# Kernel optimization log

Hardware: AMD Instinct MI355X
Metric: run time of the kernel (lower is better)

## Reference

```python
import jax, jax.numpy as jnp
import numpy as np

B, N, C = 4, 2048, 512
H = 8  # num_heads
HD = C // H  # head_dim = 64


def setup_inputs() -> dict:
    key = jax.random.key(0)
    k_x, k_qkv, k_w, k_b = jax.random.split(key, 4)
    x = jax.random.normal(k_x, (B, N, C), dtype=jnp.float32)
    # torch nn.Linear weights are stored as (out_features, in_features)
    w_qkv = jax.random.normal(k_qkv, (3 * C, C), dtype=jnp.float32) * 0.02  # bias=False
    w_proj = jax.random.normal(k_w, (C, C), dtype=jnp.float32) * 0.02
    b_proj = jax.random.normal(k_b, (C,), dtype=jnp.float32) * 0.02
    return {"x": x, "w_qkv": w_qkv, "w_proj": w_proj, "b_proj": b_proj}


def reference(x, w_qkv, w_proj, b_proj):
    b, n, c = x.shape
    scale = HD ** -0.5
    # QKV projection (no bias): (B,N,C) @ (C,3C) -> (B,N,3C)
    qkv = jnp.einsum('bnc,dc->bnd', x, w_qkv)
    qkv = qkv.reshape(b, n, 3, H, HD).transpose(2, 0, 3, 1, 4)  # (3,B,H,N,HD)
    q, k, v = qkv[0], qkv[1], qkv[2]
    # scaled dot-product attention, full N x N scores
    attn = jnp.einsum('bhqd,bhkd->bhqk', q, k) * scale
    attn = jax.nn.softmax(attn, axis=-1)
    out = jnp.einsum('bhqk,bhkd->bhqd', attn, v)  # (B,H,N,HD)
    out = out.transpose(0, 2, 1, 3).reshape(b, n, c)  # (B,N,C)
    # output projection with bias
    return jnp.einsum('bnc,dc->bnd', out, w_proj) + b_proj
```

## Files before the change

### kernel.cpp

```cpp
#include <hip/hip_runtime.h>

typedef _Float16 f16;
typedef _Float16 f16x4 __attribute__((ext_vector_type(4)));
typedef _Float16 f16x8 __attribute__((ext_vector_type(8)));
typedef __fp16 fp16x2 __attribute__((ext_vector_type(2)));
typedef float f32x4 __attribute__((ext_vector_type(4)));

static __device__ __forceinline__ f32x4 mfma_k32(f16x8 a, f16x8 b, f32x4 c) {
  return __builtin_amdgcn_mfma_f32_16x16x32_f16(a, b, c, 0, 0, 0);
}
static __device__ __forceinline__ f32x4 mfma_k16(f16x4 a, f16x4 b, f32x4 c) {
  return __builtin_amdgcn_mfma_f32_16x16x16f16(a, b, c, 0, 0, 0);
}
static __device__ __forceinline__ void gll16(const f16* g, f16* l) {
  __builtin_amdgcn_global_load_lds(
      (const __attribute__((address_space(1))) void*)g,
      (__attribute__((address_space(3))) void*)l, 16, 0, 0);
}

#define BN 2048
#define CC 512
#define NHD 64
#define MROWS 8192
#define SLAB ((size_t)32 * BN * NHD)
#define CH 64
#define QSCALE 0.1803368801111204f

__global__ __launch_bounds__(256)
void cvt_f16(const float* __restrict__ X, const float* __restrict__ Wq,
             const float* __restrict__ Wp, f16* __restrict__ x16,
             f16* __restrict__ wq16, f16* __restrict__ wp16) {
  const int idx = blockIdx.x * 256 + threadIdx.x;
  const int stride = gridDim.x * 256;
  for (int i = idx; i < (MROWS * CC) / 4; i += stride) {
    float4 v = ((const float4*)X)[i];
    f16x4 h = {(f16)v.x, (f16)v.y, (f16)v.z, (f16)v.w};
    ((f16x4*)x16)[i] = h;
  }
  for (int i = idx; i < (3 * CC * CC) / 4; i += stride) {
    float4 v = ((const float4*)Wq)[i];
    f16x4 h = {(f16)v.x, (f16)v.y, (f16)v.z, (f16)v.w};
    ((f16x4*)wq16)[i] = h;
  }
  for (int i = idx; i < (CC * CC) / 4; i += stride) {
    float4 v = ((const float4*)Wp)[i];
    f16x4 h = {(f16)v.x, (f16)v.y, (f16)v.z, (f16)v.w};
    ((f16x4*)wp16)[i] = h;
  }
}

__global__ __launch_bounds__(256)
void qkv_gemm(const f16* __restrict__ X, const f16* __restrict__ W,
              f16* __restrict__ qkv) {
  __shared__ __align__(16) f16 As[128 * 32];
  __shared__ __align__(16) f16 Bs[128 * 32];
  __shared__ __align__(16) f16 ep[64 * 130];
  const int t = threadIdx.x;
  const int lane = t & 63, wave = t >> 6;
  const int wr = wave >> 1, wc = wave & 1;
  const int mt = blockIdx.x / 12, nt = blockIdx.x % 12;
  const int m0 = mt * 128, n0 = nt * 128;
  const int grp = lane >> 4, lid = lane & 15;

  const int srow = 32 * wave + (lane >> 2);
  const int gslot = (lane & 3) ^ ((lane >> 2) & 3);
  const int ga0 = (m0 + srow) * CC + gslot * 8;
  const int gb0 = (n0 + srow) * CC + gslot * 8;
  f16* const ldsA = As + wave * 1024;
  f16* const ldsB = Bs + wave * 1024;

  const int abase = wr * 2048 + lid * 32 + (grp ^ (lid & 3)) * 8;
  const int bbase = wc * 2048 + lid * 32 + (grp ^ (lid & 3)) * 8;

  const f32x4 zf = {0.f, 0.f, 0.f, 0.f};
  f32x4 acc[4][4];
#pragma unroll
  for (int i = 0; i < 4; i++)
#pragma unroll
    for (int j = 0; j < 4; j++) acc[i][j] = zf;

  for (int k0 = 0; k0 < CC; k0 += 32) {
    gll16(X + ga0 + k0, ldsA);
    gll16(X + ga0 + 16 * CC + k0, ldsA + 512);
    gll16(W + gb0 + k0, ldsB);
    gll16(W + gb0 + 16 * CC + k0, ldsB + 512);
    __syncthreads();
    f16x8 af[4], bf[4];
#pragma unroll
    for (int mi = 0; mi < 4; mi++)
      af[mi] = *(const f16x8*)&As[abase + mi * 512];
#pragma unroll
    for (int ni = 0; ni < 4; ni++)
      bf[ni] = *(const f16x8*)&Bs[bbase + ni * 512];
#pragma unroll
    for (int mi = 0; mi < 4; mi++)
#pragma unroll
      for (int ni = 0; ni < 4; ni++)
        acc[mi][ni] = mfma_k32(af[mi], bf[ni], acc[mi][ni]);
    __syncthreads();
  }

  const int s = n0 >> 9;
  if (s == 2) {
#pragma unroll
    for (int ni = 0; ni < 4; ni++) {
      int d = n0 + wc * 64 + ni * 16 + lid;
      int h = (d & 511) >> 6;
      int hd = d & 63;
#pragma unroll
      for (int mi = 0; mi < 4; mi++) {
        int row0 = m0 + wr * 64 + mi * 16 + grp * 4;
        int b = row0 >> 11, nA = row0 & 2047;
        int posA = (nA & ~31) | (((nA >> 2) & 3) << 3) | (((nA >> 4) & 1) << 2);
        f16x4 pk = {(f16)acc[mi][ni][0], (f16)acc[mi][ni][1],
                    (f16)acc[mi][ni][2], (f16)acc[mi][ni][3]};
        *(f16x4*)&qkv[2 * SLAB + ((size_t)((b * 8 + h) * 64 + hd)) * BN + posA] = pk;
      }
    }
  } else {
    const float scale = (s == 0) ? QSCALE : 1.0f;
#pragma unroll
    for (int ph = 0; ph < 2; ++ph) {
      if (wr == ph) {
#pragma unroll
        for (int mi = 0; mi < 4; mi++)
#pragma unroll
          for (int ni = 0; ni < 4; ni++)
#pragma unroll
            for (int i = 0; i < 4; i++)
              ep[(mi * 16 + grp * 4 + i) * 130 + wc * 64 + ni * 16 + lid] =
                  (f16)(acc[mi][ni][i] * scale);
      }
      __syncthreads();
#pragma unroll
      for (int u = 0; u < 4; ++u) {
        int unit = t + u * 256;
        int row = unit >> 4, seg = unit & 15;
        int row_g = m0 + ph * 64 + row;
        int b = row_g >> 11, n = row_g & 2047;
        int d_g = n0 + seg * 8;
        int h = (d_g & 511) >> 6, hd = d_g & 63;
        f16x8 v = *(const f16x8*)&ep[row * 130 + seg * 8];
        *(f16x8*)&qkv[(size_t)s * SLAB + ((size_t)((b * 8 + h) * BN + n)) * 64 + hd] = v;
      }
      __syncthreads();
    }
  }
}

__global__ __launch_bounds__(256)
void attn(const f16* __restrict__ qkv, f16* __restrict__ O) {
  __shared__ __align__(16) char smem[32768];

  const int bh = blockIdx.x & 31;
  const int qb = blockIdx.x >> 5;
  const f16* Q = qkv + (size_t)bh * BN * NHD;
  const f16* K = qkv + SLAB + (size_t)bh * BN * NHD;
  const f16* VT = qkv + 2 * SLAB + (size_t)bh * (size_t)NHD * BN;
  const int t = threadIdx.x, lane = t & 63, wave = t >> 6;
  const int grp = lane >> 4, qv = lane & 15;
  const int qrow = qb * 64 + wave * 16 + qv;
  const int xr = (qv & 7) << 4;

  char* const kaddr0 = smem + qv * 128 + ((grp * 16) ^ xr);
  char* const kaddr1 = smem + qv * 128 + ((grp * 16 + 64) ^ xr);

  const int srow = wave * 16 + (lane >> 3);
  const int scol = (lane & 7) ^ (lane >> 3);
  const int lo_k0 = srow * NHD + scol * 8;
  const int lo_k1 = (srow + 8) * NHD + scol * 8;
  const int lo_v0 = srow * BN + scol * 8;
  const int lo_v1 = (srow + 8) * BN + scol * 8;
  f16* const dK = (f16*)(smem + wave * 2048);
  f16* const dV = (f16*)(smem + 16384 + wave * 2048);

  f16x8 qf0 = *(const f16x8*)(Q + (size_t)qrow * NHD + grp * 8);
  f16x8 qf1 = *(const f16x8*)(Q + (size_t)qrow * NHD + 32 + grp * 8);

  const f32x4 zf = {0.f, 0.f, 0.f, 0.f};
  const f16x4 ones = {(f16)1.f, (f16)1.f, (f16)1.f, (f16)1.f};
  f32x4 acc[4];
#pragma unroll
  for (int i = 0; i < 4; i++) acc[i] = zf;
  f32x4 lacc = zf;

  int koff = 0, voff = 0;
  gll16(K + lo_k0, dK);
  gll16(K + lo_k1, dK + 512);
  gll16(VT + lo_v0, dV);
  gll16(VT + lo_v1, dV + 512);
  koff = CH * NHD; voff = CH;
  __syncthreads();

#define ATTN_BODY(BUF, PF)                                                    \
  {                                                                           \
    if (PF) {                                                                 \
      gll16(K + koff + lo_k0, dK + (BUF ^ 1) * 4096);                         \
      gll16(K + koff + lo_k1, dK + (BUF ^ 1) * 4096 + 512);                   \
      gll16(VT + voff + lo_v0, dV + (BUF ^ 1) * 4096);                        \
      gll16(VT + voff + lo_v1, dV + (BUF ^ 1) * 4096 + 512);                  \
      koff += CH * NHD; voff += CH;                                           \
    }                                                                         \
    __builtin_amdgcn_s_setprio(1);                                            \
    _Pragma("unroll")                                                         \
    for (int kt2 = 0; kt2 < 2; kt2++) {                                       \
      char* const ka = kt2 ? kaddr1 : kaddr0;                                 \
      f16x8 k0a = *(const f16x8*)(kaddr0 + BUF * 8192 + kt2 * 4096);          \
      f16x8 k1a = *(const f16x8*)(kaddr1 + BUF * 8192 + kt2 * 4096);          \
      f32x4 st0 = mfma_k32(k1a, qf1, mfma_k32(k0a, qf0, zf));                 \
      f16x8 k0b = *(const f16x8*)(kaddr0 + BUF * 8192 + kt2 * 4096 + 2048);   \
      f16x8 k1b = *(const f16x8*)(kaddr1 + BUF * 8192 + kt2 * 4096 + 2048);   \
      f32x4 st1 = mfma_k32(k1b, qf1, mfma_k32(k0b, qf0, zf));                 \
      union { f16x4 v; fp16x2 h[2]; } u0, u1;                                 \
      u0.h[0] = __builtin_amdgcn_cvt_pkrtz(exp2f(st0[0]), exp2f(st0[1]));     \
      u0.h[1] = __builtin_amdgcn_cvt_pkrtz(exp2f(st0[2]), exp2f(st0[3]));     \
      u1.h[0] = __builtin_amdgcn_cvt_pkrtz(exp2f(st1[0]), exp2f(st1[1]));     \
      u1.h[1] = __builtin_amdgcn_cvt_pkrtz(exp2f(st1[2]), exp2f(st1[3]));     \
      f16x4 pb0 = u0.v, pb1 = u1.v;                                           \
      lacc = mfma_k16(ones, pb0, lacc);                                       \
      lacc = mfma_k16(ones, pb1, lacc);                                       \
      _Pragma("unroll")                                                       \
      for (int dt = 0; dt < 4; dt++) {                                        \
        union { f16x8 w; f16x4 h4[2]; } uv;                                   \
        uv.w = *(const f16x8*)(ka + 16384 + BUF * 8192 + dt * 2048);          \
        acc[dt] = mfma_k16(uv.h4[0], pb0, acc[dt]);                           \
        acc[dt] = mfma_k16(uv.h4[1], pb1, acc[dt]);                           \
      }                                                                       \
    }                                                                         \
    __builtin_amdgcn_s_setprio(0);                                            \
    __syncthreads();                                                          \
  }

  for (int p = 0; p < 15; ++p) {
    ATTN_BODY(0, 1)
    ATTN_BODY(1, 1)
  }
  ATTN_BODY(0, 1)
  ATTN_BODY(1, 0)
#undef ATTN_BODY

  const int b = bh >> 3, h = bh & 7;
  float inv = 1.0f / lacc[0];
#pragma unroll
  for (int dt = 0; dt < 4; dt++) {
    f16x4 o = {(f16)(acc[dt][0] * inv), (f16)(acc[dt][1] * inv),
               (f16)(acc[dt][2] * inv), (f16)(acc[dt][3] * inv)};
    *(f16x4*)&O[((size_t)(b * BN + qrow)) * CC + h * NHD + dt * 16 + grp * 4] = o;
  }
}

__global__ __launch_bounds__(256)
void proj_gemm(const f16* __restrict__ A, const f16* __restrict__ W,
               const float* __restrict__ bias, float* __restrict__ out) {
  __shared__ __align__(16) f16 As[128 * 32];
  __shared__ __align__(16) f16 Bs[128 * 32];
  const int t = threadIdx.x;
  const int lane = t & 63, wave = t >> 6;
  const int wr = wave >> 1, wc = wave & 1;
  const int mt = blockIdx.x >> 2, nt = blockIdx.x & 3;
  const int m0 = mt * 128, n0 = nt * 128;
  const int grp = lane >> 4, lid = lane & 15;

  const int srow = 32 * wave + (lane >> 2);
  const int gslot = (lane & 3) ^ ((lane >> 2) & 3);
  const int ga0 = (m0 + srow) * CC + gslot * 8;
  const int gb0 = (n0 + srow) * CC + gslot * 8;
  f16* const ldsA = As + wave * 1024;
  f16* const ldsB = Bs + wave * 1024;
  const int abase = wr * 2048 + lid * 32 + (grp ^ (lid & 3)) * 8;
  const int bbase = wc * 2048 + lid * 32 + (grp ^ (lid & 3)) * 8;

  const f32x4 zf = {0.f, 0.f, 0.f, 0.f};
  f32x4 acc[4][4];
#pragma unroll
  for (int i = 0; i < 4; i++)
#pragma unroll
    for (int j = 0; j < 4; j++) acc[i][j] = zf;

  for (int k0 = 0; k0 < CC; k0 += 32) {
    gll16(A + ga0 + k0, ldsA);
    gll16(A + ga0 + 16 * CC + k0, ldsA + 512);
    gll16(W + gb0 + k0, ldsB);
    gll16(W + gb0 + 16 * CC + k0, ldsB + 512);
    __syncthreads();
    f16x8 af[4], bf[4];
#pragma unroll
    for (int mi = 0; mi < 4; mi++)
      af[mi] = *(const f16x8*)&As[abase + mi * 512];
#pragma unroll
    for (int ni = 0; ni < 4; ni++)
      bf[ni] = *(const f16x8*)&Bs[bbase + ni * 512];
#pragma unroll
    for (int mi = 0; mi < 4; mi++)
#pragma unroll
      for (int ni = 0; ni < 4; ni++)
        acc[mi][ni] = mfma_k32(af[mi], bf[ni], acc[mi][ni]);
    __syncthreads();
  }
#pragma unroll
  for (int mi = 0; mi < 4; mi++) {
#pragma unroll
    for (int ni = 0; ni < 4; ni++) {
      int d = n0 + wc * 64 + ni * 16 + lid;
      float bv = bias[d];
#pragma unroll
      for (int i = 0; i < 4; i++) {
        int row = m0 + wr * 64 + mi * 16 + grp * 4 + i;
        out[(size_t)row * CC + d] = acc[mi][ni][i] + bv;
      }
    }
  }
}

extern "C" void kernel_launch(void* const* d_in, const int* in_sizes, int n_in,
                              void* d_out, int out_size, void* d_ws, size_t ws_size,
                              hipStream_t stream) {
  const float* x = (const float*)d_in[0];
  const float* w_qkv = (const float*)d_in[1];
  const float* w_proj = (const float*)d_in[2];
  const float* b_proj = (const float*)d_in[3];
  float* out = (float*)d_out;

  f16* qkv = (f16*)d_ws;
  f16* Obuf = qkv + 3 * SLAB;
  f16* x16 = Obuf;
  f16* wq16 = Obuf + (size_t)MROWS * CC;
  f16* wp16 = wq16 + (size_t)3 * CC * CC;

  cvt_f16<<<dim3(1024), dim3(256), 0, stream>>>(x, w_qkv, w_proj, x16, wq16, wp16);
  qkv_gemm<<<dim3(64 * 12), dim3(256), 0, stream>>>(x16, wq16, qkv);
  attn<<<dim3(32 * 32), dim3(256), 0, stream>>>(qkv, Obuf);
  proj_gemm<<<dim3(64 * 4), dim3(256), 0, stream>>>(Obuf, wp16, b_proj, out);
}
```

Baseline: 110.8 us.

## Stage V-transpose epilogue through LDS and halve proj GEMM M-tile

The V slab epilogue of the QKV GEMM now transposes through shared memory and writes coalesced 16-byte rows, replacing the scattered 8-byte stores into the transposed V layout. The epilogue pad changes to 136 to keep rows 16-byte aligned. The projection GEMM drops from 128x128 to 64x128 tiles and launches 512 blocks instead of 256, so more blocks can fill the CUs. This costs extra barriers in the V epilogue and less data reuse per block in the projection.

```diff
diff --git a/kernel.cpp b/kernel.cpp
--- a/kernel.cpp
+++ b/kernel.cpp
@@ -24,6 +24,7 @@
 #define MROWS 8192
 #define SLAB ((size_t)32 * BN * NHD)
 #define CH 64
+#define EPAD 136
 #define QSCALE 0.1803368801111204f
 
 __global__ __launch_bounds__(256)
@@ -54,7 +55,7 @@
               f16* __restrict__ qkv) {
   __shared__ __align__(16) f16 As[128 * 32];
   __shared__ __align__(16) f16 Bs[128 * 32];
-  __shared__ __align__(16) f16 ep[64 * 130];
+  __shared__ __align__(16) f16 ep[64 * EPAD];
   const int t = threadIdx.x;
   const int lane = t & 63, wave = t >> 6;
   const int wr = wave >> 1, wc = wave & 1;
@@ -101,21 +102,36 @@
   }
 
   const int s = n0 >> 9;
+  const int b = m0 >> 11;
+  const int nbase = m0 & 2047;
   if (s == 2) {
 #pragma unroll
-    for (int ni = 0; ni < 4; ni++) {
-      int d = n0 + wc * 64 + ni * 16 + lid;
-      int h = (d & 511) >> 6;
-      int hd = d & 63;
-#pragma unroll
-      for (int mi = 0; mi < 4; mi++) {
-        int row0 = m0 + wr * 64 + mi * 16 + grp * 4;
-        int b = row0 >> 11, nA = row0 & 2047;
-        int posA = (nA & ~31) | (((nA >> 2) & 3) << 3) | (((nA >> 4) & 1) << 2);
-        f16x4 pk = {(f16)acc[mi][ni][0], (f16)acc[mi][ni][1],
-                    (f16)acc[mi][ni][2], (f16)acc[mi][ni][3]};
-        *(f16x4*)&qkv[2 * SLAB + ((size_t)((b * 8 + h) * 64 + hd)) * BN + posA] = pk;
-      }
+    for (int ph = 0; ph < 2; ++ph) {
+      if (wc == ph) {
+#pragma unroll
+        for (int mi = 0; mi < 4; mi++) {
+          int kloc = wr * 64 + mi * 16 + grp * 4;
+          int pos = (kloc & ~31) | (grp << 3) | ((mi & 1) << 2);
+#pragma unroll
+          for (int ni = 0; ni < 4; ni++) {
+            f16x4 pk = {(f16)acc[mi][ni][0], (f16)acc[mi][ni][1],
+                        (f16)acc[mi][ni][2], (f16)acc[mi][ni][3]};
+            *(f16x4*)&ep[(ni * 16 + lid) * EPAD + pos] = pk;
+          }
+        }
+      }
+      __syncthreads();
+#pragma unroll
+      for (int u = 0; u < 4; ++u) {
+        int unit = t + u * 256;
+        int row = unit >> 4, seg = unit & 15;
+        int dg = n0 + ph * 64 + row;
+        int h = (dg & 511) >> 6, hd = dg & 63;
+        f16x8 v = *(const f16x8*)&ep[row * EPAD + seg * 8];
+        *(f16x8*)&qkv[2 * SLAB + ((size_t)((b * 8 + h) * 64 + hd)) * BN +
+                      nbase + seg * 8] = v;
+      }
+      __syncthreads();
     }
   } else {
     const float scale = (s == 0) ? QSCALE : 1.0f;
@@ -128,7 +144,7 @@
           for (int ni = 0; ni < 4; ni++)
 #pragma unroll
             for (int i = 0; i < 4; i++)
-              ep[(mi * 16 + grp * 4 + i) * 130 + wc * 64 + ni * 16 + lid] =
+              ep[(mi * 16 + grp * 4 + i) * EPAD + wc * 64 + ni * 16 + lid] =
                   (f16)(acc[mi][ni][i] * scale);
       }
       __syncthreads();
@@ -137,11 +153,12 @@
         int unit = t + u * 256;
         int row = unit >> 4, seg = unit & 15;
         int row_g = m0 + ph * 64 + row;
-        int b = row_g >> 11, n = row_g & 2047;
+        int n = row_g & 2047;
         int d_g = n0 + seg * 8;
         int h = (d_g & 511) >> 6, hd = d_g & 63;
-        f16x8 v = *(const f16x8*)&ep[row * 130 + seg * 8];
-        *(f16x8*)&qkv[(size_t)s * SLAB + ((size_t)((b * 8 + h) * BN + n)) * 64 + hd] = v;
+        f16x8 v = *(const f16x8*)&ep[row * EPAD + seg * 8];
+        *(f16x8*)&qkv[(size_t)s * SLAB +
+                      ((size_t)((b * 8 + h) * BN + n)) * 64 + hd] = v;
       }
       __syncthreads();
     }
@@ -252,60 +269,58 @@
 __global__ __launch_bounds__(256)
 void proj_gemm(const f16* __restrict__ A, const f16* __restrict__ W,
                const float* __restrict__ bias, float* __restrict__ out) {
-  __shared__ __align__(16) f16 As[128 * 32];
+  __shared__ __align__(16) f16 As[64 * 32];
   __shared__ __align__(16) f16 Bs[128 * 32];
   const int t = threadIdx.x;
   const int lane = t & 63, wave = t >> 6;
   const int wr = wave >> 1, wc = wave & 1;
   const int mt = blockIdx.x >> 2, nt = blockIdx.x & 3;
-  const int m0 = mt * 128, n0 = nt * 128;
+  const int m0 = mt * 64, n0 = nt * 128;
   const int grp = lane >> 4, lid = lane & 15;
 
-  const int srow = 32 * wave + (lane >> 2);
   const int gslot = (lane & 3) ^ ((lane >> 2) & 3);
-  const int ga0 = (m0 + srow) * CC + gslot * 8;
-  const int gb0 = (n0 + srow) * CC + gslot * 8;
-  f16* const ldsA = As + wave * 1024;
+  const int ga0 = (m0 + wave * 16 + (lane >> 2)) * CC + gslot * 8;
+  const int gb0 = (n0 + wave * 32 + (lane >> 2)) * CC + gslot * 8;
+  f16* const ldsA = As + wave * 512;
   f16* const ldsB = Bs + wave * 1024;
-  const int abase = wr * 2048 + lid * 32 + (grp ^ (lid & 3)) * 8;
-  const int bbase = wc * 2048 + lid * 32 + (grp ^ (lid & 3)) * 8;
+  const int abase = (wr * 32 + lid) * 32 + (grp ^ (lid & 3)) * 8;
+  const int bbase = (wc * 64 + lid) * 32 + (grp ^ (lid & 3)) * 8;
 
   const f32x4 zf = {0.f, 0.f, 0.f, 0.f};
-  f32x4 acc[4][4];
-#pragma unroll
-  for (int i = 0; i < 4; i++)
+  f32x4 acc[2][4];
+#pragma unroll
+  for (int i = 0; i < 2; i++)
 #pragma unroll
     for (int j = 0; j < 4; j++) acc[i][j] = zf;
 
   for (int k0 = 0; k0 < CC; k0 += 32) {
     gll16(A + ga0 + k0, ldsA);
-    gll16(A + ga0 + 16 * CC + k0, ldsA + 512);
     gll16(W + gb0 + k0, ldsB);
     gll16(W + gb0 + 16 * CC + k0, ldsB + 512);
     __syncthreads();
-    f16x8 af[4], bf[4];
-#pragma unroll
-    for (int mi = 0; mi < 4; mi++)
+    f16x8 af[2], bf[4];
+#pragma unroll
+    for (int mi = 0; mi < 2; mi++)
       af[mi] = *(const f16x8*)&As[abase + mi * 512];
 #pragma unroll
     for (int ni = 0; ni < 4; ni++)
       bf[ni] = *(const f16x8*)&Bs[bbase + ni * 512];
 #pragma unroll
-    for (int mi = 0; mi < 4; mi++)
+    for (int mi = 0; mi < 2; mi++)
 #pragma unroll
       for (int ni = 0; ni < 4; ni++)
         acc[mi][ni] = mfma_k32(af[mi], bf[ni], acc[mi][ni]);
     __syncthreads();
   }
 #pragma unroll
-  for (int mi = 0; mi < 4; mi++) {
+  for (int mi = 0; mi < 2; mi++) {
 #pragma unroll
     for (int ni = 0; ni < 4; ni++) {
       int d = n0 + wc * 64 + ni * 16 + lid;
       float bv = bias[d];
 #pragma unroll
       for (int i = 0; i < 4; i++) {
-        int row = m0 + wr * 64 + mi * 16 + grp * 4 + i;
+        int row = m0 + wr * 32 + mi * 16 + grp * 4 + i;
         out[(size_t)row * CC + d] = acc[mi][ni][i] + bv;
       }
     }
@@ -330,5 +345,5 @@
   cvt_f16<<<dim3(1024), dim3(256), 0, stream>>>(x, w_qkv, w_proj, x16, wq16, wp16);
   qkv_gemm<<<dim3(64 * 12), dim3(256), 0, stream>>>(x16, wq16, qkv);
   attn<<<dim3(32 * 32), dim3(256), 0, stream>>>(qkv, Obuf);
-  proj_gemm<<<dim3(64 * 4), dim3(256), 0, stream>>>(Obuf, wp16, b_proj, out);
-}
+  proj_gemm<<<dim3(128 * 4), dim3(256), 0, stream>>>(Obuf, wp16, b_proj, out);
+}
```

Result: faster. 104.9 us (-5.3%).
